# Kernel optimization log

Measured on AMD Instinct MI355X. Metric: run time of the kernel, lower is better.

## Reference

```python
import jax, jax.numpy as jnp
import numpy as np

V = [642, 2562, 10242]
NGT = 8000
NSAMP = 4000
CHAM_W = [3000.0, 3000.0, 3000.0]
LAP_C = [0.2, 1.0, 1.0]
CHAM_OPP = 0.55
W_LAP, W_MOVE, W_EDGE, W_NORM = 1500.0, 50.0, 359.0, 0.5


def _normalize(x, axis=-1):
    n = jnp.linalg.norm(x, axis=axis, keepdims=True)
    return x / jnp.maximum(n, 1e-12)


def _mse(a, b):
    return jnp.mean((a - b) ** 2)


def _sample_points(verts, faces, n, key):
    # uniform face pick + uniform barycentric (sqrt trick), matches sample_point_cloud
    kf, kb = jax.random.split(key)
    fidx = jax.random.randint(kf, (n,), 0, faces.shape[0])
    tri = verts[faces[fidx]]  # [n,3,3]
    uv = jax.random.uniform(kb, (n, 2), dtype=verts.dtype)
    r1 = jnp.sqrt(uv[:, 0]); r2 = uv[:, 1]
    w = jnp.stack([1.0 - r1, r1 * (1.0 - r2), r1 * r2], axis=1)  # [n,3]
    return jnp.einsum('nk,nkd->nd', w, tri)


def _chamfer(gt, pred):
    # squared pairwise distances [B,Ng,Np]
    d = (jnp.sum(gt ** 2, -1)[:, :, None] + jnp.sum(pred ** 2, -1)[:, None, :]
         - 2.0 * jnp.einsum('bnd,bmd->bnm', gt, pred))
    dist1 = jnp.min(d, 2); idx1 = jnp.argmin(d, 2)  # gt -> nearest pred
    dist2 = jnp.min(d, 1); idx2 = jnp.argmin(d, 1)  # pred -> nearest gt
    return dist1, dist2, idx1, idx2


def _laplace_coord(x, lap):
    # x [B,n,3], lap [n,10]: 8 neighbor idx (-1 invalid), self idx, count
    idx = lap[:, :8]
    mask = idx < 0
    safe = jnp.where(mask, 0, idx)
    v = x[:, safe]  # [B,n,8,3]
    v = jnp.where(mask[None, :, :, None], 0.0, v)
    cnt = lap[:, -1].astype(x.dtype)
    return x - v.sum(2) / cnt[None, :, None]


def _block(gt, gtn, pred, pred_bef, lap, edges, faces, key, cham_w, lap_c, block_idx):
    samp = _sample_points(pred[0], faces, NSAMP, key)[None]
    sample_pred = jnp.concatenate([pred, samp], 1)
    d1, d2, _i1, i2 = _chamfer(gt, sample_pred)
    chamfer = cham_w * (jnp.mean(d1) + CHAM_OPP * jnp.mean(d2))
    e = _normalize(pred[:, edges[:, 0]] - pred[:, edges[:, 1]], 2)
    nn = jnp.take_along_axis(gtn, i2[..., None], axis=1)  # nearest gt normal per pred pt
    nrm = _normalize(nn[:, edges[:, 0]], 2)
    normal = jnp.mean(jnp.abs(jnp.sum(e * nrm, 2)))
    edge = _mse(pred[:, edges[:, 0]], pred[:, edges[:, 1]]) * 3.0
    lap_l = lap_c * _mse(_laplace_coord(pred_bef, lap), _laplace_coord(pred, lap)) * 3.0
    move = lap_c * _mse(pred_bef, pred) * 3.0 if block_idx > 0 else 0.0
    return chamfer, normal, edge, lap_l, move


def setup_inputs() -> dict:
    key = jax.random.key(0)
    ks = jax.random.split(key, 8)
    inp = {}
    inp['gt_points'] = jax.random.normal(ks[0], (1, NGT, 3), jnp.float32)
    inp['gt_normals'] = _normalize(jax.random.normal(ks[1], (1, NGT, 3), jnp.float32), 2)
    for i, v in enumerate(V):
        kp, kb, ke, kf, kl = jax.random.split(ks[2 + i], 5)
        pc = jax.random.normal(kp, (1, v, 3), jnp.float32)
        inp[f'pred_coord_{i}'] = pc
        inp[f'pred_before_{i}'] = pc + 0.1 * jax.random.normal(kb, (1, v, 3), jnp.float32)
        inp[f'edges_{i}'] = jax.random.randint(ke, (3 * v, 2), 0, v, dtype=jnp.int32)
        inp[f'faces_{i}'] = jax.random.randint(kf, (2 * v, 3), 0, v, dtype=jnp.int32)
        nbr = jax.random.randint(kl, (v, 8), 0, v, dtype=jnp.int32)
        valid = (nbr % 7) != 0
        valid = valid.at[:, 0].set(True)  # count >= 1
        cnt = valid.sum(1).astype(jnp.int32)
        nbr_m = jnp.where(valid, nbr, -1)
        self_idx = jnp.arange(v, dtype=jnp.int32)[:, None]
        inp[f'lap_idx_{i}'] = jnp.concatenate([nbr_m, self_idx, cnt[:, None]], 1)
    return inp


def reference(gt_points, gt_normals,
              pred_coord_0, pred_before_0, edges_0, faces_0, lap_idx_0,
              pred_coord_1, pred_before_1, edges_1, faces_1, lap_idx_1,
              pred_coord_2, pred_before_2, edges_2, faces_2, lap_idx_2):
    skey = jax.random.key(42)
    preds = [pred_coord_0, pred_coord_1, pred_coord_2]
    befs = [pred_before_0, pred_before_1, pred_before_2]
    edges = [edges_0, edges_1, edges_2]
    faces = [faces_0, faces_1, faces_2]
    laps = [lap_idx_0, lap_idx_1, lap_idx_2]
    ch = nl = el = ll = ml = 0.0
    for i in range(3):
        c, n, e, l, m = _block(gt_points, gt_normals, preds[i], befs[i], laps[i],
                               edges[i], faces[i], jax.random.fold_in(skey, i),
                               CHAM_W[i], LAP_C[i], i)
        ch += c; nl += n; el += e; ll += l; ml += m
    loss = ch + W_LAP * ll + W_MOVE * ml + W_EDGE * el + W_NORM * nl
    return loss
```

## Files before the change

### kernel.cpp

```cpp
#include <hip/hip_runtime.h>
#include <stdint.h>

#define NGT 8000
#define NGTPAD 8064
#define NCGT 42
#define NSAMP 4000
#define QT 8
#define QB 2048
#define CH 192

struct Params {
  const float* gt;
  const float* gtn;
  const float* pred[3];
  const float* bef[3];
  const int*   edges[3];
  const int*   faces[3];
  const int*   lap[3];
  float* S[3];
  float* gtpk;
  float* Ppk[3];
  unsigned int* mb1[3];
  unsigned long long* mb2a[3];
  unsigned int* mb2b[3];
  float* acc;
  unsigned int* counter;
  unsigned int* init_base;
  int init_words;
  int prep_init_blocks;
  int v[3], M[3], E[3], F[3];
  int padM[3];
  int ppB[3];
  int cseg[10];
  int cnc[9];
  int fseg[13];
};

__device__ __forceinline__ unsigned int ford(float f){
  unsigned int b = __float_as_uint(f);
  return b ^ ((b >> 31) ? 0xFFFFFFFFu : 0x80000000u);
}
__device__ __forceinline__ float funord(unsigned int u){
  unsigned int b = u ^ ((u >> 31) ? 0x80000000u : 0xFFFFFFFFu);
  return __uint_as_float(b);
}

__device__ __forceinline__ uint32_t rotl32(uint32_t x, int d){ return (x<<d)|(x>>(32-d)); }

__device__ __forceinline__ void tf2x32(uint32_t k0, uint32_t k1, uint32_t c0, uint32_t c1,
                                       uint32_t& o0, uint32_t& o1){
  uint32_t ks2 = k0 ^ k1 ^ 0x1BD11BDAu;
  uint32_t x0 = c0 + k0, x1 = c1 + k1;
  x0+=x1; x1=rotl32(x1,13); x1^=x0;
  x0+=x1; x1=rotl32(x1,15); x1^=x0;
  x0+=x1; x1=rotl32(x1,26); x1^=x0;
  x0+=x1; x1=rotl32(x1, 6); x1^=x0;
  x0+=k1; x1+=ks2+1u;
  x0+=x1; x1=rotl32(x1,17); x1^=x0;
  x0+=x1; x1=rotl32(x1,29); x1^=x0;
  x0+=x1; x1=rotl32(x1,16); x1^=x0;
  x0+=x1; x1=rotl32(x1,24); x1^=x0;
  x0+=ks2; x1+=k0+2u;
  x0+=x1; x1=rotl32(x1,13); x1^=x0;
  x0+=x1; x1=rotl32(x1,15); x1^=x0;
  x0+=x1; x1=rotl32(x1,26); x1^=x0;
  x0+=x1; x1=rotl32(x1, 6); x1^=x0;
  x0+=k0; x1+=k1+3u;
  x0+=x1; x1=rotl32(x1,17); x1^=x0;
  x0+=x1; x1=rotl32(x1,29); x1^=x0;
  x0+=x1; x1=rotl32(x1,16); x1^=x0;
  x0+=x1; x1=rotl32(x1,24); x1^=x0;
  x0+=k1; x1+=ks2+4u;
  x0+=x1; x1=rotl32(x1,13); x1^=x0;
  x0+=x1; x1=rotl32(x1,15); x1^=x0;
  x0+=x1; x1=rotl32(x1,26); x1^=x0;
  x0+=x1; x1=rotl32(x1, 6); x1^=x0;
  x0+=ks2; x1+=k0+5u;
  o0=x0; o1=x1;
}

__device__ __forceinline__ uint32_t rbits(uint32_t k0, uint32_t k1, uint32_t idx, uint32_t total){
  uint32_t half = total>>1, o0, o1;
  if (idx < half){ tf2x32(k0,k1, idx, idx+half, o0, o1); return o0; }
  tf2x32(k0,k1, idx-half, idx, o0, o1); return o1;
}

__global__ __launch_bounds__(256) void prep_kernel(Params p){
  int b = blockIdx.x;
  int t = threadIdx.x;
  if (b < p.prep_init_blocks){
    int wdi = b*256 + t;
    if (wdi < p.init_words)
      p.init_base[wdi] = (wdi < 64) ? 0u : 0xFFFFFFFFu;
    return;
  }
  b -= p.prep_init_blocks;
  if (b < 32){
    int idx = b*256 + t;
    if (idx < NGTPAD){
      float4 o;
      if (idx < NGT){
        float x=p.gt[3*idx], y=p.gt[3*idx+1], z=p.gt[3*idx+2];
        o = make_float4(x,y,z, x*x+y*y+z*z);
      } else {
        o = make_float4(0.f,0.f,0.f,3.4e38f);
      }
      ((float4*)p.gtpk)[idx] = o;
    }
    return;
  }
  b -= 32;
  #pragma unroll
  for (int i=0;i<3;i++){
    if (b < p.ppB[i]){
      int idx = b*256 + t;
      if (idx < p.padM[i]){
        int v = p.v[i];
        if (idx < v){
          float x=p.pred[i][3*idx], y=p.pred[i][3*idx+1], z=p.pred[i][3*idx+2];
          ((float4*)p.Ppk[i])[idx] = make_float4(x,y,z, x*x+y*y+z*z);
        } else if (idx >= v + NSAMP){
          ((float4*)p.Ppk[i])[idx] = make_float4(0.f,0.f,0.f,3.4e38f);
        }
      }
      return;
    }
    b -= p.ppB[i];
  }
  int i = b >> 4;
  int s = ((b & 15) << 8) + t;
  if (s >= NSAMP) return;
  uint32_t bk0, bk1; tf2x32(0u, 42u, 0u, (uint32_t)i, bk0, bk1);
  uint32_t ka0,kb0,ka1,kb1;
  tf2x32(bk0,bk1, 0u,2u, ka0,kb0);
  tf2x32(bk0,bk1, 1u,3u, ka1,kb1);
  uint32_t fb = rbits(ka0,ka1,(uint32_t)s, NSAMP);
  uint32_t fidx = fb % (uint32_t)p.F[i];
  uint32_t u0b = rbits(kb0,kb1, 2u*(uint32_t)s,    2u*NSAMP);
  uint32_t u1b = rbits(kb0,kb1, 2u*(uint32_t)s+1u, 2u*NSAMP);
  float u0 = __uint_as_float((u0b>>9)|0x3F800000u) - 1.0f;
  float u1 = __uint_as_float((u1b>>9)|0x3F800000u) - 1.0f;
  float r1 = sqrtf(u0);
  float w0 = 1.0f - r1, w1 = r1*(1.0f-u1), w2 = r1*u1;
  const int* f = p.faces[i] + 3*(int)fidx;
  const float* pr = p.pred[i];
  int va=f[0], vb=f[1], vc=f[2];
  float d0 = w0*pr[3*va+0] + w1*pr[3*vb+0] + w2*pr[3*vc+0];
  float d1 = w0*pr[3*va+1] + w1*pr[3*vb+1] + w2*pr[3*vc+1];
  float d2 = w0*pr[3*va+2] + w1*pr[3*vb+2] + w2*pr[3*vc+2];
  float* dst = p.S[i] + 3*s;
  dst[0]=d0; dst[1]=d1; dst[2]=d2;
  ((float4*)p.Ppk[i])[p.v[i]+s] = make_float4(d0,d1,d2, d0*d0+d1*d1+d2*d2);
}


__global__ __launch_bounds__(256) void chamfer_kernel(Params p){
  int b = blockIdx.x;
  int seg = 0;
  #pragma unroll
  for (int s=1;s<9;s++) seg += (b >= p.cseg[s]) ? 1 : 0;
  int rem  = b - p.cseg[seg];
  int nc   = p.cnc[seg];
  int cq   = rem / nc;
  int cc   = rem - cq*nc;
  int role = seg / 3;
  int i    = seg - role*3;
  int t = threadIdx.x;
  int qbase = cq*QB;
  int c0 = cc*CH;
  int v = p.v[i];

  const float4* __restrict__ Pt;
  const float4* __restrict__ Qb;
  int qn, qoff;
  if (role == 0){
    Pt = (const float4*)p.Ppk[i]; Qb = (const float4*)p.gtpk;   qn = NGT;   qoff = 0;
  } else if (role == 1){
    Pt = (const float4*)p.gtpk;   Qb = (const float4*)p.Ppk[i]; qn = v;     qoff = 0;
  } else {
    Pt = (const float4*)p.gtpk;   Qb = (const float4*)p.Ppk[i]; qn = NSAMP; qoff = v;
  }
  Pt += c0;

  float qx[QT],qy[QT],qz[QT],qs[QT],best[QT];
  #pragma unroll
  for (int k=0;k<QT;k++){
    int q = qbase + t + k*256;
    float x=0.f,y=0.f,z=0.f,sv=0.f;
    if (q < qn){
      float4 g = Qb[qoff + q];
      x=g.x; y=g.y; z=g.z; sv=g.w;
    }
    qs[k]=sv; qx[k]=-2.f*x; qy[k]=-2.f*y; qz[k]=-2.f*z;
    best[k]=3.4e38f;
  }

  if (role == 1){
    int bidx[QT];
    #pragma unroll
    for (int k=0;k<QT;k++) bidx[k]=0;
    #pragma unroll 4
    for (int k=0;k<CH;k+=2){
      float4 g0 = Pt[k];
      float4 g1 = Pt[k+1];
      #pragma unroll
      for (int q=0;q<QT;q++){
        float d0 = fmaf(g0.x,qx[q], fmaf(g0.y,qy[q], fmaf(g0.z,qz[q], g0.w)));
        float d1 = fmaf(g1.x,qx[q], fmaf(g1.y,qy[q], fmaf(g1.z,qz[q], g1.w)));
        if (d0 < best[q]){ best[q]=d0; bidx[q]=c0+k;   }
        if (d1 < best[q]){ best[q]=d1; bidx[q]=c0+k+1; }
      }
    }
    #pragma unroll
    for (int k=0;k<QT;k++){
      int q = qbase + t + k*256;
      if (q < v){
        unsigned long long pk = ((unsigned long long)ford(best[k]+qs[k])<<32) | (unsigned int)bidx[k];
        atomicMin(&p.mb2a[i][q], pk);
      }
    }
  } else {
    #pragma unroll 8
    for (int k=0;k<CH;k+=2){
      float4 g0 = Pt[k];
      float4 g1 = Pt[k+1];
      #pragma unroll
      for (int q=0;q<QT;q++){
        float d0 = fmaf(g0.x,qx[q], fmaf(g0.y,qy[q], fmaf(g0.z,qz[q], g0.w)));
        float d1 = fmaf(g1.x,qx[q], fmaf(g1.y,qy[q], fmaf(g1.z,qz[q], g1.w)));
        best[q] = fminf(fminf(best[q], d0), d1);
      }
    }
    if (role == 0){
      #pragma unroll
      for (int k=0;k<QT;k++){
        int q = qbase + t + k*256;
        if (q < NGT) atomicMin(&p.mb1[i][q], ford(best[k]+qs[k]));
      }
    } else {
      #pragma unroll
      for (int k=0;k<QT;k++){
        int q = qbase + t + k*256;
        if (q < NSAMP) atomicMin(&p.mb2b[i][q], ford(best[k]+qs[k]));
      }
    }
  }
}

__global__ __launch_bounds__(256) void finish_kernel(Params p, float* out){
  __shared__ float red[256];
  int b = blockIdx.x;
  int seg = 0;
  #pragma unroll
  for (int s=1;s<12;s++) seg += (b >= p.fseg[s]) ? 1 : 0;
  int rem = b - p.fseg[seg];
  int z = seg / 3;
  int i = seg - 3*z;
  int tid = threadIdx.x;
  int gidx = rem*256 + tid;

  if (z == 0){
    int M = p.M[i], v = p.v[i];
    float val = 0.f;
    if (gidx < M){
      if (gidx < v) val = funord((unsigned int)(p.mb2a[i][gidx]>>32));
      else          val = funord(p.mb2b[i][gidx-v]);
    }
    red[tid] = val; __syncthreads();
    for (int s=128;s>0;s>>=1){ if (tid<s) red[tid]+=red[tid+s]; __syncthreads(); }
    if (tid==0 && red[0]!=0.f) atomicAdd(&p.acc[8*i+1], red[0]);
  } else if (z == 1){
    float val = 0.f;
    if (gidx < NGT) val = funord(p.mb1[i][gidx]);
    red[tid] = val; __syncthreads();
    for (int s=128;s>0;s>>=1){ if (tid<s) red[tid]+=red[tid+s]; __syncthreads(); }
    if (tid==0 && red[0]!=0.f) atomicAdd(&p.acc[8*i+0], red[0]);
  } else if (z == 2){
    int E = p.E[i];
    float sq = 0.f, ad = 0.f;
    if (gidx < E){
      int e0 = p.edges[i][2*gidx], e1 = p.edges[i][2*gidx+1];
      const float* pr = p.pred[i];
      float dx = pr[3*e0+0]-pr[3*e1+0];
      float dy = pr[3*e0+1]-pr[3*e1+1];
      float dz = pr[3*e0+2]-pr[3*e1+2];
      sq = dx*dx+dy*dy+dz*dz;
      float inv = 1.0f / fmaxf(sqrtf(sq), 1e-12f);
      int g = (int)(unsigned int)p.mb2a[i][e0];
      float nx = p.gtn[3*g+0], ny = p.gtn[3*g+1], nz = p.gtn[3*g+2];
      float invg = 1.0f / fmaxf(sqrtf(nx*nx+ny*ny+nz*nz), 1e-12f);
      ad = fabsf((dx*nx+dy*ny+dz*nz)*inv*invg);
    }
    red[tid] = ad; __syncthreads();
    for (int s=128;s>0;s>>=1){ if (tid<s) red[tid]+=red[tid+s]; __syncthreads(); }
    if (tid==0 && red[0]!=0.f) atomicAdd(&p.acc[8*i+2], red[0]);
    __syncthreads();
    red[tid] = sq; __syncthreads();
    for (int s=128;s>0;s>>=1){ if (tid<s) red[tid]+=red[tid+s]; __syncthreads(); }
    if (tid==0 && red[0]!=0.f) atomicAdd(&p.acc[8*i+3], red[0]);
  } else {
    int v = p.v[i];
    float lsq = 0.f, msq = 0.f;
    if (gidx < v){
      const int* L = p.lap[i] + 10*gidx;
      const float* B = p.bef[i];
      const float* R = p.pred[i];
      float cnt = (float)L[9];
      float sb0=0,sb1=0,sb2=0, sp0=0,sp1=0,sp2=0;
      #pragma unroll
      for (int k=0;k<8;k++){
        int id = L[k];
        if (id >= 0){
          sb0 += B[3*id+0]; sb1 += B[3*id+1]; sb2 += B[3*id+2];
          sp0 += R[3*id+0]; sp1 += R[3*id+1]; sp2 += R[3*id+2];
        }
      }
      float lb0 = B[3*gidx+0] - sb0/cnt, lb1 = B[3*gidx+1] - sb1/cnt, lb2 = B[3*gidx+2] - sb2/cnt;
      float lp0 = R[3*gidx+0] - sp0/cnt, lp1 = R[3*gidx+1] - sp1/cnt, lp2 = R[3*gidx+2] - sp2/cnt;
      float d0=lb0-lp0, d1=lb1-lp1, d2=lb2-lp2;
      lsq = d0*d0+d1*d1+d2*d2;
      float m0=B[3*gidx+0]-R[3*gidx+0], m1=B[3*gidx+1]-R[3*gidx+1], m2=B[3*gidx+2]-R[3*gidx+2];
      msq = m0*m0+m1*m1+m2*m2;
    }
    red[tid] = lsq; __syncthreads();
    for (int s=128;s>0;s>>=1){ if (tid<s) red[tid]+=red[tid+s]; __syncthreads(); }
    if (tid==0 && red[0]!=0.f) atomicAdd(&p.acc[8*i+4], red[0]);
    __syncthreads();
    red[tid] = msq; __syncthreads();
    for (int s=128;s>0;s>>=1){ if (tid<s) red[tid]+=red[tid+s]; __syncthreads(); }
    if (tid==0 && red[0]!=0.f) atomicAdd(&p.acc[8*i+5], red[0]);
  }

  __syncthreads();
  if (tid == 0){
    __threadfence();
    unsigned int total = gridDim.x;
    unsigned int old = atomicAdd(p.counter, 1u);
    if (old == total-1){
      __threadfence();
      const float CHAMW[3] = {3000.0f, 3000.0f, 3000.0f};
      const float LAPC[3]  = {0.2f, 1.0f, 1.0f};
      float loss = 0.0f;
      for (int m=0;m<3;m++){
        float a0 = __hip_atomic_load(&p.acc[8*m+0], __ATOMIC_RELAXED, __HIP_MEMORY_SCOPE_AGENT);
        float a1 = __hip_atomic_load(&p.acc[8*m+1], __ATOMIC_RELAXED, __HIP_MEMORY_SCOPE_AGENT);
        float a2 = __hip_atomic_load(&p.acc[8*m+2], __ATOMIC_RELAXED, __HIP_MEMORY_SCOPE_AGENT);
        float a3 = __hip_atomic_load(&p.acc[8*m+3], __ATOMIC_RELAXED, __HIP_MEMORY_SCOPE_AGENT);
        float a4 = __hip_atomic_load(&p.acc[8*m+4], __ATOMIC_RELAXED, __HIP_MEMORY_SCOPE_AGENT);
        float a5 = __hip_atomic_load(&p.acc[8*m+5], __ATOMIC_RELAXED, __HIP_MEMORY_SCOPE_AGENT);
        float ch = CHAMW[m]*(a0/(float)NGT + 0.55f*a1/(float)p.M[m]);
        float nl = a2/(float)p.E[m];
        float el = a3/(float)p.E[m];
        float ll = LAPC[m]*a4/(float)p.v[m];
        float ml = (m>0) ? LAPC[m]*a5/(float)p.v[m] : 0.0f;
        loss += ch + 1500.0f*ll + 50.0f*ml + 359.0f*el + 0.5f*nl;
      }
      out[0] = loss;
    }
  }
}

extern "C" void kernel_launch(void* const* d_in, const int* in_sizes, int n_in,
                              void* d_out, int out_size, void* d_ws, size_t ws_size,
                              hipStream_t stream) {
  Params p;
  p.gt  = (const float*)d_in[0];
  p.gtn = (const float*)d_in[1];
  for (int i=0;i<3;i++){
    p.pred[i]  = (const float*)d_in[2+5*i];
    p.bef[i]   = (const float*)d_in[3+5*i];
    p.edges[i] = (const int*)  d_in[4+5*i];
    p.faces[i] = (const int*)  d_in[5+5*i];
    p.lap[i]   = (const int*)  d_in[6+5*i];
    p.v[i] = in_sizes[2+5*i]/3;
    p.E[i] = in_sizes[4+5*i]/2;
    p.F[i] = in_sizes[5+5*i]/3;
    p.M[i] = p.v[i] + NSAMP;
    p.padM[i] = ((p.M[i] + CH-1)/CH)*CH;
    p.ppB[i] = (p.padM[i] + 255)/256;
  }
  unsigned int* base = (unsigned int*)d_ws;
  p.acc = (float*)base;
  p.counter = base + 32;
  p.init_base = base;
  unsigned int* w = base + 64;
  for (int i=0;i<3;i++){ p.mb1[i]  = w; w += NGT; }
  for (int i=0;i<3;i++){ p.mb2a[i] = (unsigned long long*)w; w += 2*p.v[i]; }
  for (int i=0;i<3;i++){ p.mb2b[i] = w; w += NSAMP; }
  p.init_words = (int)(w - base);
  for (int i=0;i<3;i++){ p.S[i] = (float*)w; w += NSAMP*3; }
  while ((w - base) & 3) w++;
  p.gtpk = (float*)w; w += NGTPAD*4;
  for (int i=0;i<3;i++){ p.Ppk[i] = (float*)w; w += (size_t)p.padM[i]*4; }

  int cnq[9];
  for (int i=0;i<3;i++){
    cnq[0+i] = (NGT + QB-1)/QB;           p.cnc[0+i] = p.padM[i]/CH;
    cnq[3+i] = (p.v[i] + QB-1)/QB;        p.cnc[3+i] = NCGT;
    cnq[6+i] = (NSAMP + QB-1)/QB;         p.cnc[6+i] = NCGT;
  }
  p.cseg[0] = 0;
  for (int s=0;s<9;s++) p.cseg[s+1] = p.cseg[s] + cnq[s]*p.cnc[s];

  int fn[12];
  for (int i=0;i<3;i++){
    fn[0+i] = (p.M[i] + 255)/256;
    fn[3+i] = (NGT + 255)/256;
    fn[6+i] = (p.E[i] + 255)/256;
    fn[9+i] = (p.v[i] + 255)/256;
  }
  p.fseg[0] = 0;
  for (int s=0;s<12;s++) p.fseg[s+1] = p.fseg[s] + fn[s];

  int initB = (p.init_words + 255)/256;
  p.prep_init_blocks = initB;
  int prepB = initB + 32 + p.ppB[0] + p.ppB[1] + p.ppB[2] + 3*16;

  prep_kernel   <<<dim3(prepB),     256, 0, stream>>>(p);
  chamfer_kernel<<<dim3(p.cseg[9]), 256, 0, stream>>>(p);
  finish_kernel <<<dim3(p.fseg[12]),256, 0, stream>>>(p, (float*)d_out);
}
```

Baseline: 162.1 us.

## Stream chamfer candidates via scalar s_load_dwordx16 with software prefetch, shrink CH

The chamfer inner loop now reads candidate points through explicit scalar-unit loads (s_load_dwordx16, four packed points at a time) into SGPRs, double-buffered so the next group loads while the current one is computed. This drops per-lane vector loads of uniform data and frees VGPRs. The chunk size drops from 192 to 128, giving more blocks per segment, and the unused S sample buffer and its stores are removed. The cost is more blocks and more atomicMin merges, plus inline asm with manual waitcnt and sched barriers that limit compiler scheduling.

```diff
diff --git a/kernel.cpp b/kernel.cpp
--- a/kernel.cpp
+++ b/kernel.cpp
@@ -3,11 +3,13 @@
 
 #define NGT 8000
 #define NGTPAD 8064
-#define NCGT 42
+#define NCGT 63
 #define NSAMP 4000
 #define QT 8
 #define QB 2048
-#define CH 192
+#define CH 128
+
+typedef float f32x16 __attribute__((ext_vector_type(16)));
 
 struct Params {
   const float* gt;
@@ -17,7 +19,6 @@
   const int*   edges[3];
   const int*   faces[3];
   const int*   lap[3];
-  float* S[3];
   float* gtpk;
   float* Ppk[3];
   unsigned int* mb1[3];
@@ -43,6 +44,13 @@
 __device__ __forceinline__ float funord(unsigned int u){
   unsigned int b = u ^ ((u >> 31) ? 0x80000000u : 0xFFFFFFFFu);
   return __uint_as_float(b);
+}
+
+__device__ __forceinline__ const float4* make_uniform(const float4* ptr){
+  uint64_t a = (uint64_t)ptr;
+  uint32_t lo = __builtin_amdgcn_readfirstlane((uint32_t)a);
+  uint32_t hi = __builtin_amdgcn_readfirstlane((uint32_t)(a >> 32));
+  return (const float4*)((((uint64_t)hi) << 32) | (uint64_t)lo);
 }
 
 __device__ __forceinline__ uint32_t rotl32(uint32_t x, int d){ return (x<<d)|(x>>(32-d)); }
@@ -148,11 +156,46 @@
   float d0 = w0*pr[3*va+0] + w1*pr[3*vb+0] + w2*pr[3*vc+0];
   float d1 = w0*pr[3*va+1] + w1*pr[3*vb+1] + w2*pr[3*vc+1];
   float d2 = w0*pr[3*va+2] + w1*pr[3*vb+2] + w2*pr[3*vc+2];
-  float* dst = p.S[i] + 3*s;
-  dst[0]=d0; dst[1]=d1; dst[2]=d2;
   ((float4*)p.Ppk[i])[p.v[i]+s] = make_float4(d0,d1,d2, d0*d0+d1*d1+d2*d2);
 }
 
+
+__device__ __forceinline__ void min_group(const f32x16 g,
+    const float* qx, const float* qy, const float* qz, float* best)
+{
+  #pragma unroll
+  for (int q=0;q<QT;q++){
+    float d0 = fmaf(g[0], qx[q], fmaf(g[1], qy[q], fmaf(g[2],  qz[q], g[3])));
+    float d1 = fmaf(g[4], qx[q], fmaf(g[5], qy[q], fmaf(g[6],  qz[q], g[7])));
+    float d2 = fmaf(g[8], qx[q], fmaf(g[9], qy[q], fmaf(g[10], qz[q], g[11])));
+    float d3 = fmaf(g[12],qx[q], fmaf(g[13],qy[q], fmaf(g[14], qz[q], g[15])));
+    float m = fminf(fminf(best[q], d0), d1);
+    best[q] = fminf(fminf(m, d2), d3);
+  }
+}
+
+__device__ __forceinline__ void argmin_group(const f32x16 g, int kb,
+    const float* qx, const float* qy, const float* qz, float* best, int* bidx)
+{
+  #pragma unroll
+  for (int q=0;q<QT;q++){
+    float d0 = fmaf(g[0], qx[q], fmaf(g[1], qy[q], fmaf(g[2],  qz[q], g[3])));
+    float d1 = fmaf(g[4], qx[q], fmaf(g[5], qy[q], fmaf(g[6],  qz[q], g[7])));
+    float d2 = fmaf(g[8], qx[q], fmaf(g[9], qy[q], fmaf(g[10], qz[q], g[11])));
+    float d3 = fmaf(g[12],qx[q], fmaf(g[13],qy[q], fmaf(g[14], qz[q], g[15])));
+    if (d0 < best[q]){ best[q]=d0; bidx[q]=kb+0; }
+    if (d1 < best[q]){ best[q]=d1; bidx[q]=kb+1; }
+    if (d2 < best[q]){ best[q]=d2; bidx[q]=kb+2; }
+    if (d3 < best[q]){ best[q]=d3; bidx[q]=kb+3; }
+  }
+}
+
+#define SLOAD(dst, addr) \
+  asm volatile("s_load_dwordx16 %0, %1, 0x0" : "=&s"(dst) : "s"(addr))
+#define SWAIT() do { \
+  asm volatile("s_waitcnt lgkmcnt(0)" ::: "memory"); \
+  __builtin_amdgcn_sched_barrier(0); \
+} while(0)
 
 __global__ __launch_bounds__(256) void chamfer_kernel(Params p){
   int b = blockIdx.x;
@@ -170,7 +213,7 @@
   int c0 = cc*CH;
   int v = p.v[i];
 
-  const float4* __restrict__ Pt;
+  const float4* Pt;
   const float4* __restrict__ Qb;
   int qn, qoff;
   if (role == 0){
@@ -180,7 +223,7 @@
   } else {
     Pt = (const float4*)p.gtpk;   Qb = (const float4*)p.Ppk[i]; qn = NSAMP; qoff = v;
   }
-  Pt += c0;
+  Pt = make_uniform(Pt + c0);
 
   float qx[QT],qy[QT],qz[QT],qs[QT],best[QT];
   #pragma unroll
@@ -199,18 +242,17 @@
     int bidx[QT];
     #pragma unroll
     for (int k=0;k<QT;k++) bidx[k]=0;
-    #pragma unroll 4
-    for (int k=0;k<CH;k+=2){
-      float4 g0 = Pt[k];
-      float4 g1 = Pt[k+1];
-      #pragma unroll
-      for (int q=0;q<QT;q++){
-        float d0 = fmaf(g0.x,qx[q], fmaf(g0.y,qy[q], fmaf(g0.z,qz[q], g0.w)));
-        float d1 = fmaf(g1.x,qx[q], fmaf(g1.y,qy[q], fmaf(g1.z,qz[q], g1.w)));
-        if (d0 < best[q]){ best[q]=d0; bidx[q]=c0+k;   }
-        if (d1 < best[q]){ best[q]=d1; bidx[q]=c0+k+1; }
-      }
-    }
+    f32x16 cur, nxt;
+    SLOAD(cur, Pt);
+    SWAIT();
+    #pragma unroll 2
+    for (int k=0; k<CH-4; k+=4){
+      SLOAD(nxt, Pt + k + 4);
+      argmin_group(cur, c0+k, qx,qy,qz, best, bidx);
+      SWAIT();
+      cur = nxt;
+    }
+    argmin_group(cur, c0+CH-4, qx,qy,qz, best, bidx);
     #pragma unroll
     for (int k=0;k<QT;k++){
       int q = qbase + t + k*256;
@@ -220,17 +262,17 @@
       }
     }
   } else {
-    #pragma unroll 8
-    for (int k=0;k<CH;k+=2){
-      float4 g0 = Pt[k];
-      float4 g1 = Pt[k+1];
-      #pragma unroll
-      for (int q=0;q<QT;q++){
-        float d0 = fmaf(g0.x,qx[q], fmaf(g0.y,qy[q], fmaf(g0.z,qz[q], g0.w)));
-        float d1 = fmaf(g1.x,qx[q], fmaf(g1.y,qy[q], fmaf(g1.z,qz[q], g1.w)));
-        best[q] = fminf(fminf(best[q], d0), d1);
-      }
-    }
+    f32x16 cur, nxt;
+    SLOAD(cur, Pt);
+    SWAIT();
+    #pragma unroll 2
+    for (int k=0; k<CH-4; k+=4){
+      SLOAD(nxt, Pt + k + 4);
+      min_group(cur, qx,qy,qz, best);
+      SWAIT();
+      cur = nxt;
+    }
+    min_group(cur, qx,qy,qz, best);
     if (role == 0){
       #pragma unroll
       for (int k=0;k<QT;k++){
@@ -388,7 +430,6 @@
   for (int i=0;i<3;i++){ p.mb2a[i] = (unsigned long long*)w; w += 2*p.v[i]; }
   for (int i=0;i<3;i++){ p.mb2b[i] = w; w += NSAMP; }
   p.init_words = (int)(w - base);
-  for (int i=0;i<3;i++){ p.S[i] = (float*)w; w += NSAMP*3; }
   while ((w - base) & 3) w++;
   p.gtpk = (float*)w; w += NGTPAD*4;
   for (int i=0;i<3;i++){ p.Ppk[i] = (float*)w; w += (size_t)p.padM[i]*4; }
```

Result: slower. 167.6 us (+3.3%).
